# Kernel tuning notes

Hardware: AMD Instinct MI355X
Metric: run time of the kernel (lower is better)

The kernel has to match this reference:

```python
import jax, jax.numpy as jnp
import numpy as np

BS, Q, K, NT = 16, 1500, 256, 150   # batch, queries, classes, GT per image (T = BS*NT)
COST_CLASS, COST_BBOX, COST_GIOU = 1.0, 5.0, 2.0
ALPHA, GAMMA, EPS = 0.25, 2.0, 1e-8


def box_cxcywh_to_xyxy(b):
    cx, cy, w, h = b[..., 0], b[..., 1], b[..., 2], b[..., 3]
    return jnp.stack([cx - 0.5 * w, cy - 0.5 * h, cx + 0.5 * w, cy + 0.5 * h], axis=-1)


def generalized_box_iou(boxes1, boxes2):
    # boxes in xyxy; boxes1: [N,4], boxes2: [M,4] -> [N,M]
    area1 = (boxes1[:, 2] - boxes1[:, 0]) * (boxes1[:, 3] - boxes1[:, 1])
    area2 = (boxes2[:, 2] - boxes2[:, 0]) * (boxes2[:, 3] - boxes2[:, 1])
    lt = jnp.maximum(boxes1[:, None, :2], boxes2[None, :, :2])
    rb = jnp.minimum(boxes1[:, None, 2:], boxes2[None, :, 2:])
    wh = jnp.clip(rb - lt, 0.0)
    inter = wh[..., 0] * wh[..., 1]
    union = area1[:, None] + area2[None, :] - inter
    iou = inter / union
    # smallest enclosing box
    lt_e = jnp.minimum(boxes1[:, None, :2], boxes2[None, :, :2])
    rb_e = jnp.maximum(boxes1[:, None, 2:], boxes2[None, :, 2:])
    wh_e = jnp.clip(rb_e - lt_e, 0.0)
    area_e = wh_e[..., 0] * wh_e[..., 1]
    return iou - (area_e - union) / area_e


def setup_inputs() -> dict:
    key = jax.random.key(0)
    k1, k2, k3, k4 = jax.random.split(key, 4)
    pred_logits = jax.random.normal(k1, (BS, Q, K), dtype=jnp.float32)
    pred_boxes = jax.random.uniform(k2, (BS, Q, 4), dtype=jnp.float32, minval=0.05, maxval=0.95)
    tgt_bbox = jax.random.uniform(k3, (BS * NT, 4), dtype=jnp.float32, minval=0.05, maxval=0.95)
    tgt_ids = jax.random.randint(k4, (BS * NT,), 0, K)
    return {"pred_logits": pred_logits, "pred_boxes": pred_boxes,
            "tgt_bbox": tgt_bbox, "tgt_ids": tgt_ids}


def reference(pred_logits, pred_boxes, tgt_bbox, tgt_ids):
    bs, nq, k = pred_logits.shape
    out_prob = jax.nn.sigmoid(pred_logits.reshape(bs * nq, k))   # [N, K]
    out_bbox = pred_boxes.reshape(bs * nq, 4)                    # [N, 4]

    # focal-style classification cost, gathered at target class columns
    neg_cost = (1.0 - ALPHA) * out_prob ** GAMMA * -jnp.log(1.0 - out_prob + EPS)
    pos_cost = ALPHA * (1.0 - out_prob) ** GAMMA * -jnp.log(out_prob + EPS)
    cost_class = (pos_cost - neg_cost)[:, tgt_ids]               # [N, T]

    # L1 box cost (cdist p=1)
    cost_bbox = jnp.sum(jnp.abs(out_bbox[:, None, :] - tgt_bbox[None, :, :]), axis=-1)

    # negative GIoU cost
    cost_giou = -generalized_box_iou(box_cxcywh_to_xyxy(out_bbox),
                                     box_cxcywh_to_xyxy(tgt_bbox))

    C = COST_BBOX * cost_bbox + COST_CLASS * cost_class + COST_GIOU * cost_giou
    return C.reshape(bs, nq, -1)                                  # [bs, Q, T]
```

## Files before the change

### kernel.cpp

```cpp
#include <hip/hip_runtime.h>
#include <hip/hip_fp16.h>


namespace {
constexpr int kBS = 16, kQ = 1500, kK = 256, kNT = 150;
constexpr int kT  = kBS * kNT;
constexpr int kQB = 16;
constexpr int kTT = 1024;
constexpr int kTiles = 3;
constexpr float kAlpha = 0.25f;
constexpr float kEps   = 1e-8f;
}

__global__ __launch_bounds__(256, 4)
void matcher_cost_kernel(const float* __restrict__ logits,
                         const float* __restrict__ pboxes,
                         const float* __restrict__ tboxes,
                         const int*   __restrict__ tids,
                         float* __restrict__ out)
{
    __shared__ __align__(16) __half2 s_fcl[kK][10];

    const int tid = threadIdx.x;
    const int n0  = blockIdx.x * kQB;
    const int t0  = blockIdx.y * kTT;
    const int tsz = min(kTT, kT - t0);

    const int  tbase  = t0 + (tid << 2);
    const bool active = (tid << 2) < tsz;
    float4 tb[4];
    int4 ci = make_int4(0, 0, 0, 0);
    if (active) {
        const float4* tb4 = reinterpret_cast<const float4*>(tboxes);
        ci = *reinterpret_cast<const int4*>(tids + tbase);
#pragma unroll
        for (int e = 0; e < 4; ++e) tb[e] = tb4[tbase + e];
    } else {
#pragma unroll
        for (int e = 0; e < 4; ++e) tb[e] = make_float4(0.f, 0.f, 1.f, 1.f);
    }

    {
        const float* lrow = logits + n0 * kK + tid;
#pragma unroll
        for (int qp = 0; qp < kQB / 2; ++qp) {
            float c[2];
#pragma unroll
            for (int j = 0; j < 2; ++j) {
                const float x   = lrow[(2 * qp + j) * kK];
                const float p   = __builtin_amdgcn_rcpf(1.0f + __expf(-x));
                const float omp = 1.0f - p;
                c[j] = -kAlpha * omp * omp * __logf(p + kEps)
                     + (1.0f - kAlpha) * p * p * __logf(omp + kEps) + 2.0f;
            }
            s_fcl[tid][qp] = __floats2half2_rn(c[0], c[1]);
        }
    }

    __syncthreads();
    if (!active) return;

    int   cid[4];
    float bcx[4], bcy[4], bw[4], bh[4], bx1[4], bx2[4], by1[4], by2[4], bar[4];
    cid[0] = ci.x; cid[1] = ci.y; cid[2] = ci.z; cid[3] = ci.w;
#pragma unroll
    for (int e = 0; e < 4; ++e) {
        bcx[e] = tb[e].x; bcy[e] = tb[e].y; bw[e] = tb[e].z; bh[e] = tb[e].w;
        bx1[e] = bcx[e] - 0.5f * bw[e];  bx2[e] = bcx[e] + 0.5f * bw[e];
        by1[e] = bcy[e] - 0.5f * bh[e];  by2[e] = bcy[e] + 0.5f * bh[e];
        bar[e] = bw[e] * bh[e];
    }

    float* __restrict__ orow = out + (size_t)n0 * kT + tbase;

#pragma unroll
    for (int qg = 0; qg < 4; ++qg) {
        uint2 ccr[4];
#pragma unroll
        for (int e = 0; e < 4; ++e)
            ccr[e] = *reinterpret_cast<const uint2*>(&s_fcl[cid[e]][qg * 2]);

#pragma unroll
        for (int qi = 0; qi < 4; ++qi) {
            const int q = qg * 4 + qi;
            const float4 pb = *reinterpret_cast<const float4*>(pboxes + (n0 + q) * 4);
            const float pcx = pb.x, pcy = pb.y, pw = pb.z, ph = pb.w;
            const float px1 = pcx - 0.5f * pw, px2 = pcx + 0.5f * pw;
            const float py1 = pcy - 0.5f * ph, py2 = pcy + 0.5f * ph;
            const float parea = pw * ph;

            float res[4];
#pragma unroll
            for (int e = 0; e < 4; ++e) {
                const unsigned u   = (qi < 2) ? ccr[e].x : ccr[e].y;
                const __half2  h2  = *reinterpret_cast<const __half2*>(&u);
                const float ccp2   = (qi & 1) ? __high2float(h2) : __low2float(h2);
                const float cb = fabsf(pcx - bcx[e]) + fabsf(pcy - bcy[e])
                               + fabsf(pw  - bw[e])  + fabsf(ph  - bh[e]);
                const float ow = fminf(px2, bx2[e]) - fmaxf(px1, bx1[e]);
                const float oh = fminf(py2, by2[e]) - fmaxf(py1, by1[e]);
                const float iw = fmaxf(ow, 0.0f), ih = fmaxf(oh, 0.0f);
                const float ew = (pw + bw[e]) - ow, eh = (ph + bh[e]) - oh;
                const float inter = iw * ih;
                const float uni   = (parea + bar[e]) - inter;
                const float ear   = ew * eh;
                const float rr   = __builtin_amdgcn_rcpf(uni * ear);
                const float frac = fmaf(uni, uni, inter * ear) * rr;
                res[e] = fmaf(5.0f, cb, ccp2) - 2.0f * frac;
            }
            *reinterpret_cast<float4*>(orow + (size_t)q * kT) =
                make_float4(res[0], res[1], res[2], res[3]);
        }
    }
}

extern "C" void kernel_launch(void* const* d_in, const int* in_sizes, int n_in,
                              void* d_out, int out_size, void* d_ws, size_t ws_size,
                              hipStream_t stream) {
    const float* logits = (const float*)d_in[0];
    const float* pboxes = (const float*)d_in[1];
    const float* tboxes = (const float*)d_in[2];
    const int*   tids   = (const int*)d_in[3];
    float* out = (float*)d_out;

    dim3 grid(kBS * kQ / kQB, kTiles);
    dim3 block(256);
    hipLaunchKernelGGL(matcher_cost_kernel, grid, block, 0, stream,
                       logits, pboxes, tboxes, tids, out);
}
```

Measured before the change: 269.6 us.

## Cover all targets per block with fewer queries and nontemporal stores

Drops the 2D grid over target tiles. Each block now takes 8 queries and loops over all 2400 targets in three passes, so the sigmoid/focal cost table is built once per query block instead of once per target tile, removing duplicated logit loads and transcendental work. Output writes use nontemporal stores to avoid polluting cache with the large write-only cost matrix. A few fma contractions are also added. Each block does more serial work and reloads target boxes per pass, and the last pass leaves most threads idle.

```diff
diff --git a/kernel.cpp b/kernel.cpp
--- a/kernel.cpp
+++ b/kernel.cpp
@@ -4,12 +4,12 @@
 
 namespace {
 constexpr int kBS = 16, kQ = 1500, kK = 256, kNT = 150;
-constexpr int kT  = kBS * kNT;
-constexpr int kQB = 16;
-constexpr int kTT = 1024;
-constexpr int kTiles = 3;
+constexpr int kT   = kBS * kNT;
+constexpr int kN   = kBS * kQ;
+constexpr int kQB  = 8;
 constexpr float kAlpha = 0.25f;
 constexpr float kEps   = 1e-8f;
+typedef float floatx4 __attribute__((ext_vector_type(4)));
 }
 
 __global__ __launch_bounds__(256, 4)
@@ -19,29 +19,13 @@
                          const int*   __restrict__ tids,
                          float* __restrict__ out)
 {
-    __shared__ __align__(16) __half2 s_fcl[kK][10];
+    __shared__ __align__(16) __half2 s_fcl[kK][6];
 
     const int tid = threadIdx.x;
     const int n0  = blockIdx.x * kQB;
-    const int t0  = blockIdx.y * kTT;
-    const int tsz = min(kTT, kT - t0);
-
-    const int  tbase  = t0 + (tid << 2);
-    const bool active = (tid << 2) < tsz;
-    float4 tb[4];
-    int4 ci = make_int4(0, 0, 0, 0);
-    if (active) {
-        const float4* tb4 = reinterpret_cast<const float4*>(tboxes);
-        ci = *reinterpret_cast<const int4*>(tids + tbase);
-#pragma unroll
-        for (int e = 0; e < 4; ++e) tb[e] = tb4[tbase + e];
-    } else {
-#pragma unroll
-        for (int e = 0; e < 4; ++e) tb[e] = make_float4(0.f, 0.f, 1.f, 1.f);
-    }
 
     {
-        const float* lrow = logits + n0 * kK + tid;
+        const float* lrow = logits + (size_t)n0 * kK + tid;
 #pragma unroll
         for (int qp = 0; qp < kQB / 2; ++qp) {
             float c[2];
@@ -56,62 +40,69 @@
             s_fcl[tid][qp] = __floats2half2_rn(c[0], c[1]);
         }
     }
+    __syncthreads();
 
-    __syncthreads();
-    if (!active) return;
+    const float4* __restrict__ tb4 = reinterpret_cast<const float4*>(tboxes);
 
-    int   cid[4];
-    float bcx[4], bcy[4], bw[4], bh[4], bx1[4], bx2[4], by1[4], by2[4], bar[4];
-    cid[0] = ci.x; cid[1] = ci.y; cid[2] = ci.z; cid[3] = ci.w;
+    auto tilework = [&](int tbase) {
+        const int4 ci = *reinterpret_cast<const int4*>(tids + tbase);
+        const int cid[4] = {ci.x, ci.y, ci.z, ci.w};
+        float bcx[4], bcy[4], bw[4], bh[4], bx1[4], bx2[4], by1[4], by2[4];
 #pragma unroll
-    for (int e = 0; e < 4; ++e) {
-        bcx[e] = tb[e].x; bcy[e] = tb[e].y; bw[e] = tb[e].z; bh[e] = tb[e].w;
-        bx1[e] = bcx[e] - 0.5f * bw[e];  bx2[e] = bcx[e] + 0.5f * bw[e];
-        by1[e] = bcy[e] - 0.5f * bh[e];  by2[e] = bcy[e] + 0.5f * bh[e];
-        bar[e] = bw[e] * bh[e];
-    }
-
-    float* __restrict__ orow = out + (size_t)n0 * kT + tbase;
+        for (int e = 0; e < 4; ++e) {
+            const float4 b = tb4[tbase + e];
+            bcx[e] = b.x; bcy[e] = b.y; bw[e] = b.z; bh[e] = b.w;
+            bx1[e] = fmaf(-0.5f, bw[e], bcx[e]);  bx2[e] = fmaf(0.5f, bw[e], bcx[e]);
+            by1[e] = fmaf(-0.5f, bh[e], bcy[e]);  by2[e] = fmaf(0.5f, bh[e], bcy[e]);
+        }
+        float* __restrict__ ob = out + (size_t)n0 * kT + tbase;
 
 #pragma unroll
-    for (int qg = 0; qg < 4; ++qg) {
-        uint2 ccr[4];
+        for (int qg = 0; qg < kQB / 4; ++qg) {
+            uint2 ccr[4];
 #pragma unroll
-        for (int e = 0; e < 4; ++e)
-            ccr[e] = *reinterpret_cast<const uint2*>(&s_fcl[cid[e]][qg * 2]);
+            for (int e = 0; e < 4; ++e)
+                ccr[e] = *reinterpret_cast<const uint2*>(&s_fcl[cid[e]][qg * 2]);
 
 #pragma unroll
-        for (int qi = 0; qi < 4; ++qi) {
-            const int q = qg * 4 + qi;
-            const float4 pb = *reinterpret_cast<const float4*>(pboxes + (n0 + q) * 4);
-            const float pcx = pb.x, pcy = pb.y, pw = pb.z, ph = pb.w;
-            const float px1 = pcx - 0.5f * pw, px2 = pcx + 0.5f * pw;
-            const float py1 = pcy - 0.5f * ph, py2 = pcy + 0.5f * ph;
-            const float parea = pw * ph;
+            for (int qi = 0; qi < 4; ++qi) {
+                const int q = qg * 4 + qi;
+                const float4 pb = *reinterpret_cast<const float4*>(
+                                      pboxes + (size_t)(n0 + q) * 4);
+                const float pcx = pb.x, pcy = pb.y, pw = pb.z, ph = pb.w;
+                const float px1 = fmaf(-0.5f, pw, pcx), px2 = fmaf(0.5f, pw, pcx);
+                const float py1 = fmaf(-0.5f, ph, pcy), py2 = fmaf(0.5f, ph, pcy);
+                const float parea = pw * ph;
 
-            float res[4];
+                floatx4 res;
 #pragma unroll
-            for (int e = 0; e < 4; ++e) {
-                const unsigned u   = (qi < 2) ? ccr[e].x : ccr[e].y;
-                const __half2  h2  = *reinterpret_cast<const __half2*>(&u);
-                const float ccp2   = (qi & 1) ? __high2float(h2) : __low2float(h2);
-                const float cb = fabsf(pcx - bcx[e]) + fabsf(pcy - bcy[e])
-                               + fabsf(pw  - bw[e])  + fabsf(ph  - bh[e]);
-                const float ow = fminf(px2, bx2[e]) - fmaxf(px1, bx1[e]);
-                const float oh = fminf(py2, by2[e]) - fmaxf(py1, by1[e]);
-                const float iw = fmaxf(ow, 0.0f), ih = fmaxf(oh, 0.0f);
-                const float ew = (pw + bw[e]) - ow, eh = (ph + bh[e]) - oh;
-                const float inter = iw * ih;
-                const float uni   = (parea + bar[e]) - inter;
-                const float ear   = ew * eh;
-                const float rr   = __builtin_amdgcn_rcpf(uni * ear);
-                const float frac = fmaf(uni, uni, inter * ear) * rr;
-                res[e] = fmaf(5.0f, cb, ccp2) - 2.0f * frac;
+                for (int e = 0; e < 4; ++e) {
+                    const unsigned u  = (qi < 2) ? ccr[e].x : ccr[e].y;
+                    const __half2 h2  = *reinterpret_cast<const __half2*>(&u);
+                    const float   cc  = (qi & 1) ? __high2float(h2) : __low2float(h2);
+                    const float cb = fabsf(pcx - bcx[e]) + fabsf(pcy - bcy[e])
+                                   + fabsf(pw - bw[e])  + fabsf(ph - bh[e]);
+                    const float ow = fminf(px2, bx2[e]) - fmaxf(px1, bx1[e]);
+                    const float oh = fminf(py2, by2[e]) - fmaxf(py1, by1[e]);
+                    const float iw = fmaxf(ow, 0.0f), ih = fmaxf(oh, 0.0f);
+                    const float ew = (pw + bw[e]) - ow, eh = (ph + bh[e]) - oh;
+                    const float inter = iw * ih;
+                    const float uni   = fmaf(bw[e], bh[e], parea) - inter;
+                    const float ear   = ew * eh;
+                    const float rr   = __builtin_amdgcn_rcpf(uni * ear);
+                    const float frac = fmaf(uni, uni, inter * ear) * rr;
+                    res[e] = fmaf(-2.0f, frac, fmaf(5.0f, cb, cc));
+                }
+                __builtin_nontemporal_store(
+                    res, reinterpret_cast<floatx4*>(ob + (size_t)q * kT));
             }
-            *reinterpret_cast<float4*>(orow + (size_t)q * kT) =
-                make_float4(res[0], res[1], res[2], res[3]);
         }
-    }
+    };
+
+    const int o4 = tid << 2;
+    tilework(o4);
+    tilework(1024 + o4);
+    if (o4 < 352) tilework(2048 + o4);
 }
 
 extern "C" void kernel_launch(void* const* d_in, const int* in_sizes, int n_in,
@@ -123,7 +114,7 @@
     const int*   tids   = (const int*)d_in[3];
     float* out = (float*)d_out;
 
-    dim3 grid(kBS * kQ / kQB, kTiles);
+    dim3 grid(kN / kQB);
     dim3 block(256);
     hipLaunchKernelGGL(matcher_cost_kernel, grid, block, 0, stream,
                        logits, pboxes, tboxes, tids, out);
```

After: 266.9 us. Within noise of the previous version (-1.0%).
